# Performance work log

Hardware: AMD Instinct MI355X
Metric: run time of the kernel (lower is better)

The kernel has to match this reference:

```python
import jax, jax.numpy as jnp
import numpy as np

N_NODES = 25000
N_EDGES = 250000
F_IN = 32
F_OUT = 32
EDGE_DIM = 6
H1, H2 = 64, 128


def setup_inputs() -> dict:
    key = jax.random.key(0)
    ks = jax.random.split(key, 10)
    s = 0.05
    return {
        "x": jax.random.normal(ks[0], (N_NODES, F_IN), dtype=jnp.float32),
        "edge_attr": jax.random.normal(ks[1], (N_EDGES, EDGE_DIM), dtype=jnp.float32),
        # fnet MLP params: Linear(6->64), ReLU, Linear(64->128), ReLU, Linear(128->F_IN*F_OUT)
        "W1": jax.random.normal(ks[2], (H1, EDGE_DIM), dtype=jnp.float32) * s,
        "b1": jnp.zeros((H1,), dtype=jnp.float32),
        "W2": jax.random.normal(ks[3], (H2, H1), dtype=jnp.float32) * s,
        "b2": jnp.zeros((H2,), dtype=jnp.float32),
        "W3": jax.random.normal(ks[4], (F_IN * F_OUT, H2), dtype=jnp.float32) * s,
        "b3": jnp.zeros((F_IN * F_OUT,), dtype=jnp.float32),
        "edge_src": jax.random.randint(ks[5], (N_EDGES,), 0, N_NODES),
        "edge_dst": jax.random.randint(ks[6], (N_EDGES,), 0, N_NODES),
    }


def reference(x, edge_attr, W1, b1, W2, b2, W3, b3, edge_src, edge_dst):
    # fnet: per-edge MLP producing a dynamic filter theta_e of shape [F_OUT, F_IN]
    h = jax.nn.relu(edge_attr @ W1.T + b1)            # [E, H1]
    h = jax.nn.relu(h @ W2.T + b2)                    # [E, H2]
    theta = (h @ W3.T + b3).reshape(-1, F_OUT, F_IN)  # [E, F_OUT, F_IN]
    # gather source features, apply per-edge filter
    msg = jnp.einsum('eoi,ei->eo', theta, x[edge_src])  # [E, F_OUT]
    # scatter-mean over destination nodes (ECC averages over neighborhood)
    agg = jax.ops.segment_sum(msg, edge_dst, num_segments=N_NODES)
    deg = jax.ops.segment_sum(jnp.ones((msg.shape[0],), x.dtype), edge_dst,
                              num_segments=N_NODES)
    out = agg / jnp.maximum(deg, 1.0)[:, None]        # [N, F_OUT]
    return jax.nn.relu(out)                           # trailing 'r' in config
```

## Files before the change

### kernel.cpp

```cpp
#include <hip/hip_runtime.h>
#include <hip/hip_fp16.h>

#define N_NODES 25000
#define N_EDGES 250000
#define ED 6
#define H1 64
#define H2 128
#define NBLK 977
#define NCHUNK 33
#define CHUNK_USH 4096
#define W3S_USHORTS (NCHUNK*CHUNK_USH)
#define W2S_USHORTS (H2*H1)
#define SCAN_BLOCKS 98

typedef float f32x4 __attribute__((ext_vector_type(4)));
typedef float f32x16 __attribute__((ext_vector_type(16)));
typedef _Float16 f16x8 __attribute__((ext_vector_type(8)));
typedef __fp16 fp16x2 __attribute__((ext_vector_type(2)));
typedef unsigned int u32x4 __attribute__((ext_vector_type(4)));
typedef unsigned int u32x2 __attribute__((ext_vector_type(2)));

union F16x8U { u32x4 u; f16x8 h; };
union PKU    { fp16x2 p; unsigned u; };
union HU     { unsigned short u; _Float16 h; };

__device__ __forceinline__ unsigned pkrtz(float lo, float hi) {
    PKU r; r.p = __builtin_amdgcn_cvt_pkrtz(lo, hi); return r.u;
}
__device__ __forceinline__ unsigned pk_mul_blo(unsigned h, unsigned x) {
    unsigned d;
    asm("v_pk_mul_f16 %0, %1, %2 op_sel:[0,0] op_sel_hi:[0,1]" : "=v"(d) : "v"(h), "v"(x));
    return d;
}
__device__ __forceinline__ unsigned pk_mul_bhi(unsigned h, unsigned x) {
    unsigned d;
    asm("v_pk_mul_f16 %0, %1, %2 op_sel:[1,0] op_sel_hi:[1,1]" : "=v"(d) : "v"(h), "v"(x));
    return d;
}
__device__ __forceinline__ f32x4 mfma16(f16x8 a, f16x8 b, f32x4 c) {
    return __builtin_amdgcn_mfma_f32_16x16x32_f16(a, b, c, 0, 0, 0);
}
__device__ __forceinline__ f32x16 mfma32(f16x8 a, f16x8 b, f32x16 c) {
    return __builtin_amdgcn_mfma_f32_32x32x16_f16(a, b, c, 0, 0, 0);
}
__device__ __forceinline__ void gload16(const void* g, void* l) {
    __builtin_amdgcn_global_load_lds(
        (const __attribute__((address_space(1))) unsigned int*)g,
        (__attribute__((address_space(3))) unsigned int*)l, 16, 0, 0);
}

__global__ __launch_bounds__(256) void ecc_init(
    const float* __restrict__ W3, const float* __restrict__ b3,
    const float* __restrict__ W2,
    unsigned* __restrict__ cnt, unsigned short* __restrict__ w3s,
    unsigned short* __restrict__ w2s, float* __restrict__ agg)
{
    int idx = blockIdx.x * 256 + threadIdx.x;
    if (idx < W3S_USHORTS) {
        int c = idx >> 12, r = idx & 4095;
        int ks = r >> 9;
        int lane = (r >> 3) & 63;
        int j = r & 7;
        int o = lane & 31;
        int kp = c * 128 + ks * 16 + ((lane >> 5) << 3) + j;
        float v = 0.f;
        if (kp < 4096)      { int k = kp >> 5, i = kp & 31; v = W3[(o * 32 + i) * 128 + k]; }
        else if (kp < 4128) { v = b3[o * 32 + (kp - 4096)]; }
        __half hv = __float2half_rn(v);
        w3s[idx] = *reinterpret_cast<unsigned short*>(&hv);
    }
    if (idx < W2S_USHORTS) {
        __half hv = __float2half_rn(W2[idx]);
        w2s[idx] = *reinterpret_cast<unsigned short*>(&hv);
    }
    if (idx < N_NODES) cnt[idx] = 0u;
    if (idx < N_NODES * 32) agg[idx] = 0.f;
}

__global__ __launch_bounds__(256) void ecc_hist(
    const int* __restrict__ dst, unsigned* __restrict__ cnt,
    unsigned* __restrict__ rank)
{
    int e = blockIdx.x * 256 + threadIdx.x;
    if (e < N_EDGES) rank[e] = atomicAdd(&cnt[dst[e]], 1u);
}

__global__ __launch_bounds__(256) void ecc_scan1(
    const unsigned* __restrict__ cnt, unsigned* __restrict__ off,
    unsigned* __restrict__ bsum)
{
    __shared__ unsigned s[256];
    const int t = threadIdx.x, i = blockIdx.x * 256 + t;
    unsigned v = (i < N_NODES) ? cnt[i] : 0u;
    s[t] = v; __syncthreads();
    #pragma unroll
    for (int d = 1; d < 256; d <<= 1) {
        unsigned add = (t >= d) ? s[t - d] : 0u;
        __syncthreads(); s[t] += add; __syncthreads();
    }
    if (i < N_NODES) off[i] = s[t] - v;
    if (t == 255) bsum[blockIdx.x] = s[255];
}

__global__ __launch_bounds__(128) void ecc_scan2(
    const unsigned* __restrict__ bsum, unsigned* __restrict__ bsumx)
{
    __shared__ unsigned s[128];
    const int t = threadIdx.x;
    unsigned v = (t < SCAN_BLOCKS) ? bsum[t] : 0u;
    s[t] = v; __syncthreads();
    #pragma unroll
    for (int d = 1; d < 128; d <<= 1) {
        unsigned add = (t >= d) ? s[t - d] : 0u;
        __syncthreads(); s[t] += add; __syncthreads();
    }
    if (t < SCAN_BLOCKS) bsumx[t] = s[t] - v;
}

__global__ __launch_bounds__(256) void ecc_scan3(
    unsigned* __restrict__ off, const unsigned* __restrict__ bsumx)
{
    int i = blockIdx.x * 256 + threadIdx.x;
    if (i < N_NODES) off[i] += bsumx[blockIdx.x];
    if (i == 0) off[N_NODES] = N_EDGES;
}

__global__ __launch_bounds__(256) void ecc_perm(
    const int* __restrict__ dst, const unsigned* __restrict__ off,
    const unsigned* __restrict__ rank, unsigned* __restrict__ perm,
    int* __restrict__ bfirst)
{
    int e = blockIdx.x * 256 + threadIdx.x;
    if (e < N_EDGES) perm[off[dst[e]] + rank[e]] = (unsigned)e;
    if (e < NBLK) {
        const unsigned tile = (unsigned)e * 256u;
        int loN = 0, hiN = N_NODES;
        while (loN < hiN) {
            int mid = (loN + hiN) >> 1;
            if (off[mid + 1] > tile) hiN = mid; else loN = mid + 1;
        }
        bfirst[e] = loN;
    }
}

__global__ __launch_bounds__(256) void ecc_fused(
    const float* __restrict__ x,   const float* __restrict__ ea,
    const float* __restrict__ W1,  const float* __restrict__ b1,
    const unsigned short* __restrict__ w2s, const float* __restrict__ b2,
    const unsigned short* __restrict__ w3s,
    const int* __restrict__ src,   const unsigned* __restrict__ perm,
    const unsigned* __restrict__ off, const int* __restrict__ bfirst,
    float* __restrict__ agg)
{
    __shared__ __align__(16) unsigned short sm[256 * H2];
    __shared__ __align__(16) unsigned short wbuf[2][CHUNK_USH];

    const int t = threadIdx.x;
    const int tile = blockIdx.x * 256;
    const int slot = tile + t;
    const bool ev = (slot < N_EDGES);
    const unsigned je = ev ? perm[slot] : 0u;

    const int w = t >> 6, l = t & 63, lr = l & 15, kg = l >> 4;
    const int l31 = l & 31, l5 = l >> 5;

    gload16(w3s + t * 8,        &wbuf[0][t * 8]);
    gload16(w3s + 2048 + t * 8, &wbuf[0][2048 + t * 8]);

    {
        float a[ED];
        #pragma unroll
        for (int c = 0; c < ED; ++c) a[c] = ev ? ea[(long)je * ED + c] : 0.f;

        float h1[H1];
        #pragma unroll
        for (int o = 0; o < H1; ++o) {
            float acc = b1[o];
            #pragma unroll
            for (int c = 0; c < ED; ++c) acc = fmaf(W1[o * ED + c], a[c], acc);
            h1[o] = fmaxf(acc, 0.f);
        }
        #pragma unroll
        for (int q = 0; q < 8; ++q) {
            u32x4 pk;
            #pragma unroll
            for (int j = 0; j < 4; ++j)
                pk[j] = pkrtz(h1[q*8 + 2*j], h1[q*8 + 2*j + 1]);
            const int boff = (t * 128 + q * 16) ^ ((t & 7) << 4);
            *(u32x4*)((char*)sm + boff) = pk;
        }
    }

    unsigned xsh[2][8];
    #pragma unroll
    for (int mt = 0; mt < 2; ++mt) {
        const int er = tile + w * 64 + mt * 32 + l31;
        if (er < N_EDGES) {
            const float* xb = x + (long)src[perm[er]] * 32;
            const float4* xp = (const float4*)(xb + l5 * 8);
            const float4* xq = (const float4*)(xb + 16 + l5 * 8);
            float4 v0 = xp[0], v1 = xp[1], v2 = xq[0], v3 = xq[1];
            xsh[mt][0] = pkrtz(v0.x, v0.y); xsh[mt][1] = pkrtz(v0.z, v0.w);
            xsh[mt][2] = pkrtz(v1.x, v1.y); xsh[mt][3] = pkrtz(v1.z, v1.w);
            xsh[mt][4] = pkrtz(v2.x, v2.y); xsh[mt][5] = pkrtz(v2.z, v2.w);
            xsh[mt][6] = pkrtz(v3.x, v3.y); xsh[mt][7] = pkrtz(v3.z, v3.w);
        } else {
            #pragma unroll
            for (int j = 0; j < 8; ++j) xsh[mt][j] = 0u;
        }
    }

    {
        F16x8U hb[4][2];
        #pragma unroll
        for (int ne = 0; ne < 4; ++ne) {
            const int er = w * 64 + ne * 16 + lr;
            #pragma unroll
            for (int ks = 0; ks < 2; ++ks) {
                const int boff = (er * 128 + ks * 64 + kg * 16) ^ ((er & 7) << 4);
                hb[ne][ks].u = *(const u32x4*)((const char*)sm + boff);
            }
        }
        __syncthreads();

        #pragma unroll
        for (int mo = 0; mo < 8; ++mo) {
            F16x8U a2[2];
            #pragma unroll
            for (int ks = 0; ks < 2; ++ks)
                a2[ks].u = *(const u32x4*)(w2s + (mo*16 + lr) * 64 + ks*32 + kg*8);
            const float4 bv = *(const float4*)(b2 + mo*16 + kg*4);
            #pragma unroll
            for (int ne = 0; ne < 4; ++ne) {
                f32x4 c = (f32x4){0.f, 0.f, 0.f, 0.f};
                c = mfma16(a2[0].h, hb[ne][0].h, c);
                c = mfma16(a2[1].h, hb[ne][1].h, c);
                const unsigned p0 = pkrtz(fmaxf(c[0]+bv.x, 0.f), fmaxf(c[1]+bv.y, 0.f));
                const unsigned p1 = pkrtz(fmaxf(c[2]+bv.z, 0.f), fmaxf(c[3]+bv.w, 0.f));
                const int er = w * 64 + ne * 16 + lr;
                const int boff = (er * 256 + (mo*16 + kg*4) * 2) ^ ((er & 7) << 4);
                *(u32x2*)((char*)sm + boff) = (u32x2){p0, p1};
            }
        }
    }

    f32x16 acc[2];
    #pragma unroll
    for (int i = 0; i < 16; ++i) { acc[0][i] = 0.f; acc[1][i] = 0.f; }

    __syncthreads();

    int cur = 0;
    #pragma unroll 1
    for (int c = 0; c < 32; ++c) {
        {
            const unsigned short* gs = w3s + (c + 1) * CHUNK_USH + t * 8;
            gload16(gs,        &wbuf[cur ^ 1][t * 8]);
            gload16(gs + 2048, &wbuf[cur ^ 1][2048 + t * 8]);
        }
        const char* wb = (const char*)wbuf[cur] + l * 16;

        u32x2 hv[2];
        #pragma unroll
        for (int mt = 0; mt < 2; ++mt) {
            const int row = w * 64 + mt * 32 + l31;
            const int boff = (row * 256 + c * 8) ^ ((row & 7) << 4);
            hv[mt] = *(const u32x2*)((const char*)sm + boff);
        }

        __builtin_amdgcn_s_setprio(1);
        #pragma unroll
        for (int ks = 0; ks < 8; ++ks) {
            F16x8U bf;
            bf.u = *(const u32x4*)(wb + ks * 1024);
            const int kl = ks >> 1;
            const int xb = (ks & 1) * 4;
            #pragma unroll
            for (int mt = 0; mt < 2; ++mt) {
                const unsigned h01 = hv[mt][kl >> 1];
                F16x8U af;
                if (kl & 1) {
                    af.u[0] = pk_mul_bhi(h01, xsh[mt][xb + 0]);
                    af.u[1] = pk_mul_bhi(h01, xsh[mt][xb + 1]);
                    af.u[2] = pk_mul_bhi(h01, xsh[mt][xb + 2]);
                    af.u[3] = pk_mul_bhi(h01, xsh[mt][xb + 3]);
                } else {
                    af.u[0] = pk_mul_blo(h01, xsh[mt][xb + 0]);
                    af.u[1] = pk_mul_blo(h01, xsh[mt][xb + 1]);
                    af.u[2] = pk_mul_blo(h01, xsh[mt][xb + 2]);
                    af.u[3] = pk_mul_blo(h01, xsh[mt][xb + 3]);
                }
                acc[mt] = mfma32(af.h, bf.h, acc[mt]);
            }
        }
        __builtin_amdgcn_s_setprio(0);

        __syncthreads();
        cur ^= 1;
    }
    {
        const char* wb = (const char*)wbuf[cur] + l * 16;
        F16x8U bf0, bf1;
        bf0.u = *(const u32x4*)(wb);
        bf1.u = *(const u32x4*)(wb + 1024);
        #pragma unroll
        for (int mt = 0; mt < 2; ++mt) {
            F16x8U af;
            af.u = (u32x4){xsh[mt][0], xsh[mt][1], xsh[mt][2], xsh[mt][3]};
            acc[mt] = mfma32(af.h, bf0.h, acc[mt]);
            af.u = (u32x4){xsh[mt][4], xsh[mt][5], xsh[mt][6], xsh[mt][7]};
            acc[mt] = mfma32(af.h, bf1.h, acc[mt]);
        }
    }

    __syncthreads();
    {
        unsigned short* msgl = (unsigned short*)sm;
        #pragma unroll
        for (int mt = 0; mt < 2; ++mt) {
            #pragma unroll
            for (int rg = 0; rg < 16; ++rg) {
                const int el = w * 64 + mt * 32 + (rg & 3) + 8 * (rg >> 2) + 4 * l5;
                HU hv; hv.h = (_Float16)acc[mt][rg];
                msgl[el * 32 + l31] = hv.u;
            }
        }
    }
    __syncthreads();

    {
        const unsigned short* msgl = (const unsigned short*)sm;
        const int n0 = bfirst[blockIdx.x];
        const int tend = tile + 256;
        #pragma unroll 1
        for (int p = t; ; p += 256) {
            const int n = n0 + (p >> 5);
            if (n >= N_NODES) break;
            const unsigned lo = off[n], hi = off[n + 1];
            if ((int)lo >= tend) break;
            const int o = p & 31;
            const int jb = max((int)lo, tile), jend = min((int)hi, tend);
            if (jend > jb) {
                float s = 0.f;
                for (int j = jb; j < jend; ++j) {
                    HU v; v.u = msgl[(j - tile) * 32 + o];
                    s += (float)v.h;
                }
                atomicAdd(&agg[(long)n * 32 + o], s);
            }
        }
    }
}

__global__ __launch_bounds__(256) void ecc_finalize(
    const float* __restrict__ agg, const unsigned* __restrict__ cnt,
    float* __restrict__ out)
{
    const int i = blockIdx.x * 256 + threadIdx.x;
    if (i >= N_NODES * 32) return;
    const int n = i >> 5;
    const float d = fmaxf((float)cnt[n], 1.f);
    out[i] = fmaxf(agg[i] / d, 0.f);
}

extern "C" void kernel_launch(void* const* d_in, const int* in_sizes, int n_in,
                              void* d_out, int out_size, void* d_ws, size_t ws_size,
                              hipStream_t stream) {
    const float* x   = (const float*)d_in[0];
    const float* ea  = (const float*)d_in[1];
    const float* W1  = (const float*)d_in[2];
    const float* b1  = (const float*)d_in[3];
    const float* W2  = (const float*)d_in[4];
    const float* b2  = (const float*)d_in[5];
    const float* W3  = (const float*)d_in[6];
    const float* b3  = (const float*)d_in[7];
    const int*   src = (const int*)d_in[8];
    const int*   dst = (const int*)d_in[9];
    float* out = (float*)d_out;

    char* p = (char*)d_ws;
    unsigned short* w3s = (unsigned short*)p; p += W3S_USHORTS * 2;
    unsigned short* w2s = (unsigned short*)p; p += 16384;
    unsigned* cnt   = (unsigned*)p; p += 100096;
    unsigned* off   = (unsigned*)p; p += 100352;
    unsigned* bsum  = (unsigned*)p; p += 512;
    unsigned* bsumx = (unsigned*)p; p += 512;
    int*      bfirst= (int*)p;      p += 4096;
    unsigned* rank  = (unsigned*)p; p += 1000192;
    unsigned* perm  = (unsigned*)p; p += 1000192;
    float*    agg   = (float*)p;

    ecc_init<<<(N_NODES * 32 + 255) / 256, 256, 0, stream>>>(W3, b3, W2, cnt, w3s, w2s, agg);
    ecc_hist<<<NBLK, 256, 0, stream>>>(dst, cnt, rank);
    ecc_scan1<<<SCAN_BLOCKS, 256, 0, stream>>>(cnt, off, bsum);
    ecc_scan2<<<1, 128, 0, stream>>>(bsum, bsumx);
    ecc_scan3<<<SCAN_BLOCKS, 256, 0, stream>>>(off, bsumx);
    ecc_perm<<<NBLK, 256, 0, stream>>>(dst, off, rank, perm, bfirst);
    ecc_fused<<<NBLK, 256, 0, stream>>>(x, ea, W1, b1, w2s, b2, w3s, src, perm, off, bfirst, agg);
    ecc_finalize<<<(N_NODES * 32 + 255) / 256, 256, 0, stream>>>(agg, cnt, out);
}
```

Baseline: 125.9 us.

## Split K across wave pairs so each wave reuses W3 fragments over more edges

The main contraction loop changes its work split. Each pair of waves now covers 128 edges, and the two waves in a pair take different halves of the K dimension within each chunk. Each W3 fragment loaded from LDS is therefore reused across four edge tiles instead of two, which halves the LDS weight reads per MFMA. The cost is twice as many accumulator registers and x-fragment registers, which may reduce occupancy. A cross-wave reduction is also added: partial sums go to LDS in fp32 and are summed during the segment reduction.

```diff
diff --git a/kernel.cpp b/kernel.cpp
--- a/kernel.cpp
+++ b/kernel.cpp
@@ -22,7 +22,6 @@
 
 union F16x8U { u32x4 u; f16x8 h; };
 union PKU    { fp16x2 p; unsigned u; };
-union HU     { unsigned short u; _Float16 h; };
 
 __device__ __forceinline__ unsigned pkrtz(float lo, float hi) {
     PKU r; r.p = __builtin_amdgcn_cvt_pkrtz(lo, hi); return r.u;
@@ -163,6 +162,8 @@
 
     const int w = t >> 6, l = t & 63, lr = l & 15, kg = l >> 4;
     const int l31 = l & 31, l5 = l >> 5;
+    const int epair  = w >> 1;
+    const int kshalf = w & 1;
 
     gload16(w3s + t * 8,        &wbuf[0][t * 8]);
     gload16(w3s + 2048 + t * 8, &wbuf[0][2048 + t * 8]);
@@ -191,10 +192,10 @@
         }
     }
 
-    unsigned xsh[2][8];
+    unsigned xsh[4][8];
     #pragma unroll
-    for (int mt = 0; mt < 2; ++mt) {
-        const int er = tile + w * 64 + mt * 32 + l31;
+    for (int mt = 0; mt < 4; ++mt) {
+        const int er = tile + epair * 128 + mt * 32 + l31;
         if (er < N_EDGES) {
             const float* xb = x + (long)src[perm[er]] * 32;
             const float4* xp = (const float4*)(xb + l5 * 8);
@@ -244,9 +245,11 @@
         }
     }
 
-    f32x16 acc[2];
+    f32x16 acc[4];
     #pragma unroll
-    for (int i = 0; i < 16; ++i) { acc[0][i] = 0.f; acc[1][i] = 0.f; }
+    for (int mt = 0; mt < 4; ++mt)
+        #pragma unroll
+        for (int i = 0; i < 16; ++i) acc[mt][i] = 0.f;
 
     __syncthreads();
 
@@ -258,37 +261,35 @@
             gload16(gs,        &wbuf[cur ^ 1][t * 8]);
             gload16(gs + 2048, &wbuf[cur ^ 1][2048 + t * 8]);
         }
-        const char* wb = (const char*)wbuf[cur] + l * 16;
-
-        u32x2 hv[2];
-        #pragma unroll
-        for (int mt = 0; mt < 2; ++mt) {
-            const int row = w * 64 + mt * 32 + l31;
-            const int boff = (row * 256 + c * 8) ^ ((row & 7) << 4);
-            hv[mt] = *(const u32x2*)((const char*)sm + boff);
+        const char* wb = (const char*)wbuf[cur] + kshalf * 4096 + l * 16;
+
+        unsigned hv[4];
+        #pragma unroll
+        for (int mt = 0; mt < 4; ++mt) {
+            const int row = epair * 128 + mt * 32 + l31;
+            const int boff = (row * 256 + c * 8 + kshalf * 4) ^ ((row & 7) << 4);
+            hv[mt] = *(const unsigned*)((const char*)sm + boff);
         }
 
         __builtin_amdgcn_s_setprio(1);
         #pragma unroll
-        for (int ks = 0; ks < 8; ++ks) {
+        for (int ks = 0; ks < 4; ++ks) {
             F16x8U bf;
             bf.u = *(const u32x4*)(wb + ks * 1024);
-            const int kl = ks >> 1;
             const int xb = (ks & 1) * 4;
             #pragma unroll
-            for (int mt = 0; mt < 2; ++mt) {
-                const unsigned h01 = hv[mt][kl >> 1];
+            for (int mt = 0; mt < 4; ++mt) {
                 F16x8U af;
-                if (kl & 1) {
-                    af.u[0] = pk_mul_bhi(h01, xsh[mt][xb + 0]);
-                    af.u[1] = pk_mul_bhi(h01, xsh[mt][xb + 1]);
-                    af.u[2] = pk_mul_bhi(h01, xsh[mt][xb + 2]);
-                    af.u[3] = pk_mul_bhi(h01, xsh[mt][xb + 3]);
+                if (ks & 2) {
+                    af.u[0] = pk_mul_bhi(hv[mt], xsh[mt][xb + 0]);
+                    af.u[1] = pk_mul_bhi(hv[mt], xsh[mt][xb + 1]);
+                    af.u[2] = pk_mul_bhi(hv[mt], xsh[mt][xb + 2]);
+                    af.u[3] = pk_mul_bhi(hv[mt], xsh[mt][xb + 3]);
                 } else {
-                    af.u[0] = pk_mul_blo(h01, xsh[mt][xb + 0]);
-                    af.u[1] = pk_mul_blo(h01, xsh[mt][xb + 1]);
-                    af.u[2] = pk_mul_blo(h01, xsh[mt][xb + 2]);
-                    af.u[3] = pk_mul_blo(h01, xsh[mt][xb + 3]);
+                    af.u[0] = pk_mul_blo(hv[mt], xsh[mt][xb + 0]);
+                    af.u[1] = pk_mul_blo(hv[mt], xsh[mt][xb + 1]);
+                    af.u[2] = pk_mul_blo(hv[mt], xsh[mt][xb + 2]);
+                    af.u[3] = pk_mul_blo(hv[mt], xsh[mt][xb + 3]);
                 }
                 acc[mt] = mfma32(af.h, bf.h, acc[mt]);
             }
@@ -298,13 +299,13 @@
         __syncthreads();
         cur ^= 1;
     }
-    {
+    if (kshalf == 0) {
         const char* wb = (const char*)wbuf[cur] + l * 16;
         F16x8U bf0, bf1;
         bf0.u = *(const u32x4*)(wb);
         bf1.u = *(const u32x4*)(wb + 1024);
         #pragma unroll
-        for (int mt = 0; mt < 2; ++mt) {
+        for (int mt = 0; mt < 4; ++mt) {
             F16x8U af;
             af.u = (u32x4){xsh[mt][0], xsh[mt][1], xsh[mt][2], xsh[mt][3]};
             acc[mt] = mfma32(af.h, bf0.h, acc[mt]);
@@ -315,21 +316,20 @@
 
     __syncthreads();
     {
-        unsigned short* msgl = (unsigned short*)sm;
-        #pragma unroll
-        for (int mt = 0; mt < 2; ++mt) {
+        float* pm = (float*)sm;
+        #pragma unroll
+        for (int mt = 0; mt < 4; ++mt) {
             #pragma unroll
             for (int rg = 0; rg < 16; ++rg) {
-                const int el = w * 64 + mt * 32 + (rg & 3) + 8 * (rg >> 2) + 4 * l5;
-                HU hv; hv.h = (_Float16)acc[mt][rg];
-                msgl[el * 32 + l31] = hv.u;
+                const int el = epair * 128 + mt * 32 + (rg & 3) + 8 * (rg >> 2) + 4 * l5;
+                pm[kshalf * 8192 + el * 32 + l31] = acc[mt][rg];
             }
         }
     }
     __syncthreads();
 
     {
-        const unsigned short* msgl = (const unsigned short*)sm;
+        const float* pm = (const float*)sm;
         const int n0 = bfirst[blockIdx.x];
         const int tend = tile + 256;
         #pragma unroll 1
@@ -343,8 +343,8 @@
             if (jend > jb) {
                 float s = 0.f;
                 for (int j = jb; j < jend; ++j) {
-                    HU v; v.u = msgl[(j - tile) * 32 + o];
-                    s += (float)v.h;
+                    const int jl = j - tile;
+                    s += pm[jl * 32 + o] + pm[8192 + jl * 32 + o];
                 }
                 atomicAdd(&agg[(long)n * 32 + o], s);
             }
```

New measurement: 129.8 us. +3.0%, slower.
